# Kernel tuning notes

Hardware: AMD Instinct MI355X
Metric: run time of the kernel (lower is better)

Reference implementation:

```python
import jax, jax.numpy as jnp
import numpy as np

CLS_THR = 0.7      # cls_threshold
NMS_THR = 0.7      # nms_threshold
MAX_OUT = 100      # nms_max_outputs
MIN_SIZE = 3.0     # min_size_threshold


def setup_inputs() -> dict:
    key = jax.random.key(0)
    k1, k2 = jax.random.split(key)
    B, H, W, A = 1, 128, 128, 9
    img_h = img_w = 2048
    # build valid pixel-space boxes [y1,x1,y2,x2] with y2>y1, x2>x1
    r = jax.random.uniform(k1, (B, H, W, A, 4), dtype=jnp.float32)
    y1 = r[..., 0] * (img_h - 200.0)
    x1 = r[..., 1] * (img_w - 200.0)
    y2 = y1 + 1.0 + r[..., 2] * 199.0
    x2 = x1 + 1.0 + r[..., 3] * 199.0
    proposals = jnp.stack([y1, x1, y2, x2], axis=-1).reshape(B, H, W, A * 4)
    cls_score = jax.random.normal(k2, (B, H, W, A * 2), dtype=jnp.float32) * 2.0
    return {"proposals": proposals, "cls_score": cls_score,
            "image_h": img_h, "image_w": img_w}


def reference(proposals, cls_score, image_h, image_w):
    B, H, W = proposals.shape[0], proposals.shape[1], proposals.shape[2]
    A = proposals.shape[3] // 4
    boxes = proposals.reshape(-1, 4)                       # [N,4] yxyx, pixels
    prob = jax.nn.softmax(cls_score.reshape(B, H, W, A, 2), axis=-1)
    score0 = prob[..., 0].reshape(-1)                      # [N] objectness
    # threshold mask (tf boolean_mask replaced by fixed-shape invalidation)
    active0 = jnp.where(score0 > CLS_THR, score0, -1.0)
    areas = (boxes[:, 2] - boxes[:, 0]) * (boxes[:, 3] - boxes[:, 1])

    def nms_step(active, _):
        idx = jnp.argmax(active)
        ok = active[idx] > 0.0                             # any box left?
        b = boxes[idx]
        yy1 = jnp.maximum(b[0], boxes[:, 0])
        xx1 = jnp.maximum(b[1], boxes[:, 1])
        yy2 = jnp.minimum(b[2], boxes[:, 2])
        xx2 = jnp.minimum(b[3], boxes[:, 3])
        inter = jnp.maximum(yy2 - yy1, 0.0) * jnp.maximum(xx2 - xx1, 0.0)
        iou = inter / (areas + areas[idx] - inter + 1e-9)
        active = jnp.where(iou > NMS_THR, -1.0, active)
        active = active.at[idx].set(-1.0)
        return active, (idx, ok)

    _, (idxs, oks) = jax.lax.scan(nms_step, active0, None, length=MAX_OUT)
    sel_boxes = boxes[idxs]                                # [100,4]
    sel_cls = score0[idxs]                                 # [100]
    # remove_small_proposals: h,w from yxyx -> yxhw
    hgt = sel_boxes[:, 2] - sel_boxes[:, 0]
    wid = sel_boxes[:, 3] - sel_boxes[:, 1]
    keep = oks & (hgt > MIN_SIZE) & (wid > MIN_SIZE)
    sel_boxes = jnp.where(keep[:, None], sel_boxes, 0.0)
    sel_cls = jnp.where(keep, sel_cls, 0.0)
    # format == 'percentage': exact pixel coords -> fraction of image
    scale = jnp.array([image_h, image_w, image_h, image_w], dtype=jnp.float32)
    sel_boxes = (sel_boxes / scale)[None]                  # [1,100,4]
    return sel_boxes, sel_cls[None]                        # [1,100]
```

## Files before the change

### kernel.cpp

```cpp
#include <hip/hip_runtime.h>


#define CLS_THR 0.7f
#define NMS_THR 0.7f
#define MAX_OUT 100
#define MIN_SZ  3.0f

#define N_CAP      147456
#define BASE_BITS  0x3F333334u
#define BIN_SHIFT  9
#define NBINS      9831
#define HIST_WORDS 10240
#define PAD_WORD   10000
#define CTR_WORD   10100
#define TARGET     160u
#define CAP        512
#define CHUNK      128
#define BUCKET_NB  1024
#define BUCKET_LO  (NBINS - BUCKET_NB)
#define BCAP       64

__device__ __forceinline__ float softmax0(float l0, float l1) {
    float m  = fmaxf(l0, l1);
    float e0 = expf(l0 - m);
    float e1 = expf(l1 - m);
    return e0 / (e0 + e1);
}

__device__ __forceinline__ unsigned int ld_dev_u32(const unsigned int* p) {
    return __hip_atomic_load(p, __ATOMIC_RELAXED, __HIP_MEMORY_SCOPE_AGENT);
}
__device__ __forceinline__ unsigned long long ld_dev_u64(const unsigned long long* p) {
    return __hip_atomic_load(p, __ATOMIC_RELAXED, __HIP_MEMORY_SCOPE_AGENT);
}
__device__ __forceinline__ void st_dev_u64(unsigned long long* p, unsigned long long v) {
    __hip_atomic_store(p, v, __ATOMIC_RELAXED, __HIP_MEMORY_SCOPE_AGENT);
}
__device__ __forceinline__ unsigned long long pack2f(float a, float b) {
    return ((unsigned long long)__float_as_uint(b) << 32) | __float_as_uint(a);
}

__launch_bounds__(256)
__global__ void fused_kernel(const float4* __restrict__ boxes,
                             const float4* __restrict__ cls,
                             unsigned int* hist,
                             unsigned long long* bucket,
                             const int* __restrict__ ph, const int* __restrict__ pw,
                             float* __restrict__ out, int N, int nblocks)
{
    __shared__ unsigned long long s_kbuf[CAP];
    __shared__ unsigned long long s_sorted[CAP];
    __shared__ float4 s_bbox[CAP];
    __shared__ unsigned int s_binof[CAP];
    __shared__ unsigned int s_sup[CHUNK][4];
    __shared__ unsigned int s_rowflag[4];
    __shared__ unsigned int s_seedm[4];
    __shared__ unsigned int s_keep[4];
    __shared__ unsigned int s_gpack[CAP];
    __shared__ unsigned int s_goff[CAP];
    __shared__ unsigned int s_wsum[4];
    __shared__ float  s_klist[MAX_OUT][5];
    __shared__ float4 s_kbox[MAX_OUT];
    __shared__ float  s_karea[MAX_OUT];
    __shared__ int s_cbin, s_ov, s_kept, s_ne, s_last, s_cutT;
    __shared__ unsigned int s_M, s_cnt;

    const int tid  = threadIdx.x;
    const int lane = tid & 63;
    const int wave = tid >> 6;

    const unsigned int X = hist[PAD_WORD];

    {
        int t = blockIdx.x * 256 + tid;
        int i = t * 2;
        if (i < N) {
            float4 v  = cls[t];
            float4 b0 = boxes[i];
            float4 b1 = (i + 1 < N) ? boxes[i + 1] : b0;
            float p0 = softmax0(v.x, v.y);
            float p1 = (i + 1 < N) ? softmax0(v.z, v.w) : 0.0f;
            if (p0 > CLS_THR) {
                unsigned int b = __float_as_uint(p0);
                int bin = (int)((b - BASE_BITS) >> BIN_SHIFT);
                unsigned int slot = atomicAdd(&hist[bin], 1u) - X;
                if (bin >= BUCKET_LO && slot < BCAP) {
                    size_t ba = ((size_t)(bin - BUCKET_LO) * BCAP + slot) * 3;
                    st_dev_u64(&bucket[ba],
                        ((unsigned long long)b << 32) | (unsigned int)(~i));
                    st_dev_u64(&bucket[ba + 1], pack2f(b0.x, b0.y));
                    st_dev_u64(&bucket[ba + 2], pack2f(b0.z, b0.w));
                }
            }
            if (p1 > CLS_THR) {
                unsigned int b = __float_as_uint(p1);
                int bin = (int)((b - BASE_BITS) >> BIN_SHIFT);
                unsigned int slot = atomicAdd(&hist[bin], 1u) - X;
                if (bin >= BUCKET_LO && slot < BCAP) {
                    size_t ba = ((size_t)(bin - BUCKET_LO) * BCAP + slot) * 3;
                    st_dev_u64(&bucket[ba],
                        ((unsigned long long)b << 32) | (unsigned int)(~(i + 1)));
                    st_dev_u64(&bucket[ba + 1], pack2f(b1.x, b1.y));
                    st_dev_u64(&bucket[ba + 2], pack2f(b1.z, b1.w));
                }
            }
        }
    }
    asm volatile("s_waitcnt vmcnt(0)" ::: "memory");
    __syncthreads();
    if (tid == 0) {
        unsigned int old = atomicAdd(&hist[CTR_WORD], 1u);
        s_last = (old - X == (unsigned int)(nblocks - 1)) ? 1 : 0;
    }
    __syncthreads();
    if (!s_last) return;

    const float img_h = (float)(*ph);
    const float img_w = (float)(*pw);

    int kept = 0;
    int hi = NBINS;
    bool done = false;

    while (!done) {
        if (tid == 0) { s_cutT = -1; s_ov = 0; s_cnt = 0u; s_ne = 0; }
        __syncthreads();

        bool usefast = false;
        unsigned int h_reg = 0u, cum_reg = 0u;

        if (hi == NBINS) {
            int b = NBINS - 1 - tid;
            h_reg = ld_dev_u32(&hist[b]) - X;
            unsigned int pref = h_reg;
            #pragma unroll
            for (int o = 1; o < 64; o <<= 1) {
                unsigned int t2 = __shfl_up(pref, o);
                if (lane >= o) pref += t2;
            }
            if (lane == 63) s_wsum[wave] = pref;
            __syncthreads();
            unsigned int cum = pref;
            for (int q = 0; q < wave; ++q) cum += s_wsum[q];
            cum_reg = cum;
            if (cum >= TARGET && cum - h_reg < TARGET) {
                s_cutT = tid; s_M = cum; s_cbin = b;
            }
            __syncthreads();
            int cutT = s_cutT;
            if (cutT >= 0) {
                if (tid <= cutT && h_reg > BCAP) s_ov = 1;
                __syncthreads();
                usefast = (!s_ov) && (s_M <= 256u);
                if (usefast) {
                    if (tid <= cutT && h_reg > 0u) {
                        unsigned int off = cum_reg - h_reg;
                        unsigned int rb  = (unsigned int)(NBINS - 1 - tid - BUCKET_LO);
                        for (unsigned int s = 0; s < h_reg; ++s)
                            if (off + s < CAP) s_binof[off + s] = (rb << 6) | s;
                    }
                    __syncthreads();
                    unsigned int M = s_M;
                    unsigned long long key = 0ull;
                    float4 bx = make_float4(0.f, 0.f, 0.f, 0.f);
                    if ((unsigned int)tid < M) {
                        unsigned int bs = s_binof[tid];
                        size_t ba = ((size_t)(bs >> 6) * BCAP + (bs & 63u)) * 3;
                        key = ld_dev_u64(&bucket[ba]);
                        unsigned long long w1 = ld_dev_u64(&bucket[ba + 1]);
                        unsigned long long w2 = ld_dev_u64(&bucket[ba + 2]);
                        bx.x = __uint_as_float((unsigned int)w1);
                        bx.y = __uint_as_float((unsigned int)(w1 >> 32));
                        bx.z = __uint_as_float((unsigned int)w2);
                        bx.w = __uint_as_float((unsigned int)(w2 >> 32));
                        s_kbuf[tid] = key;
                    }
                    __syncthreads();
                    if ((unsigned int)tid < M) {
                        unsigned int rank = 0u;
                        #pragma unroll 8
                        for (unsigned int j = 0; j < M; ++j)
                            rank += (s_kbuf[j] > key) ? 1u : 0u;
                        s_sorted[rank] = key;
                        s_bbox[rank]   = bx;
                    }
                    __syncthreads();
                }
            } else {
                __syncthreads();
            }
        }

        if (!usefast) {
            if (wave == 0) {
                int pos = hi; unsigned int run = 0u; int cb = -1;
                unsigned int M = 0u; int ov = 0;
                while (pos > 0) {
                    int b = pos - 1 - lane;
                    unsigned int h = (b >= 0) ? (ld_dev_u32(&hist[b]) - X) : 0u;
                    unsigned int pref = h;
                    #pragma unroll
                    for (int o = 1; o < 64; o <<= 1) {
                        unsigned int t2 = __shfl_up(pref, o);
                        if (lane >= o) pref += t2;
                    }
                    unsigned int cum = run + pref;
                    unsigned long long okm = __ballot(b >= 0 && cum >= TARGET);
                    unsigned long long ovm = __ballot(b >= 0 && h > BCAP);
                    if (okm) {
                        int first = __builtin_ctzll(okm);
                        cb = pos - 1 - first;
                        M  = __shfl(cum, first);
                        unsigned long long lm = (first >= 63) ? ~0ull
                                              : ((1ull << (first + 1)) - 1ull);
                        if (ovm & lm) ov = 1;
                        break;
                    }
                    if (ovm) ov = 1;
                    run += __shfl(pref, 63);
                    pos -= 64;
                }
                if (cb < 0) { cb = 0; M = run; }
                if (lane == 0) { s_cbin = cb; s_M = M; s_ov = ov; }
            }
            __syncthreads();
        }

        const int cbin = s_cbin;
        const unsigned int M = s_M;
        if (M == 0u) break;
        const unsigned int M_eff = (M > CAP) ? CAP : M;

        if (!usefast) {
            const bool usebucket = (!s_ov) && (cbin >= BUCKET_LO);
            if (usebucket) {
                if (wave == 0) {
                    int pos = hi; unsigned int run = 0u; int ne = 0;
                    while (pos > cbin) {
                        int b = pos - 1 - lane;
                        unsigned int h = (b >= cbin) ? (ld_dev_u32(&hist[b]) - X) : 0u;
                        unsigned int pref = h;
                        #pragma unroll
                        for (int o = 1; o < 64; o <<= 1) {
                            unsigned int t2 = __shfl_up(pref, o);
                            if (lane >= o) pref += t2;
                        }
                        unsigned int offv = run + pref - h;
                        unsigned long long nzm = __ballot(h > 0u);
                        int slot = ne + __popcll(nzm & ((1ull << lane) - 1ull));
                        if (h > 0u && slot < CAP) {
                            s_gpack[slot] = ((unsigned int)b << 16) | h;
                            s_goff[slot]  = offv;
                        }
                        ne  += __popcll(nzm);
                        run += __shfl(pref, 63);
                        pos -= 64;
                    }
                    if (lane == 0) s_ne = ne;
                }
                __syncthreads();
                int ne = s_ne; if (ne > CAP) ne = CAP;
                for (int e = wave; e < ne; e += 4) {
                    unsigned int pk = s_gpack[e];
                    int b = (int)(pk >> 16);
                    unsigned int cnt = pk & 0xFFFFu;
                    unsigned int off = s_goff[e];
                    if (lane < (int)cnt && off + lane < CAP)
                        s_kbuf[off + lane] = ld_dev_u64(
                            &bucket[((size_t)(b - BUCKET_LO) * BCAP + lane) * 3]);
                }
            } else {
                unsigned int th_lo = BASE_BITS + ((unsigned int)cbin << BIN_SHIFT);
                unsigned int th_hi = BASE_BITS + ((unsigned int)hi   << BIN_SHIFT);
                int NV = N >> 1;
                for (int basei = 0; basei < NV; basei += 256 * 8) {
                    float4 v[8];
                    #pragma unroll
                    for (int u = 0; u < 8; ++u) {
                        int i4 = basei + u * 256 + tid;
                        v[u] = (i4 < NV) ? cls[i4]
                                         : make_float4(0.f, 0.f, 0.f, 0.f);
                    }
                    #pragma unroll
                    for (int u = 0; u < 8; ++u) {
                        int i0 = (basei + u * 256 + tid) * 2;
                        float p0 = softmax0(v[u].x, v[u].y);
                        float p1 = softmax0(v[u].z, v[u].w);
                        if (p0 > CLS_THR) {
                            unsigned int b = __float_as_uint(p0);
                            if (b >= th_lo && b < th_hi) {
                                unsigned int sl = atomicAdd(&s_cnt, 1u);
                                if (sl < CAP)
                                    s_kbuf[sl] = ((unsigned long long)b << 32)
                                               | (unsigned int)(~i0);
                            }
                        }
                        if (p1 > CLS_THR) {
                            unsigned int b = __float_as_uint(p1);
                            if (b >= th_lo && b < th_hi) {
                                unsigned int sl = atomicAdd(&s_cnt, 1u);
                                if (sl < CAP)
                                    s_kbuf[sl] = ((unsigned long long)b << 32)
                                               | (unsigned int)(~(i0 + 1));
                            }
                        }
                    }
                }
            }
            __syncthreads();
            for (unsigned int t = tid; t < M_eff; t += 256) {
                unsigned long long kt = s_kbuf[t];
                unsigned int rank = 0u;
                #pragma unroll 8
                for (unsigned int j = 0; j < M_eff; ++j)
                    rank += (s_kbuf[j] > kt) ? 1u : 0u;
                s_sorted[rank] = kt;
            }
            __syncthreads();
            for (unsigned int t = tid; t < M_eff; t += 256) {
                int idx = (int)(~(unsigned int)s_sorted[t]);
                s_bbox[t] = boxes[idx];
            }
            __syncthreads();
        }

        int base = 0;
        while (base < (int)M_eff && kept < MAX_OUT) {
            int C = (int)M_eff - base; if (C > CHUNK) C = CHUNK;
            if (tid < CHUNK) { s_sup[tid][0] = 0u; s_sup[tid][1] = 0u;
                               s_sup[tid][2] = 0u; s_sup[tid][3] = 0u; }
            if (tid < 4) { s_rowflag[tid] = 0u; s_seedm[tid] = 0u;
                           s_keep[tid] = 0u; }
            __syncthreads();

            if (kept > 0 && (tid & 127) < C) {
                int i = tid & 127;
                float4 cb = s_bbox[base + i];
                float ca = (cb.z - cb.x) * (cb.w - cb.y);
                bool sup = false;
                for (int j = (tid >> 7); j < kept; j += 2) {
                    float4 kb = s_kbox[j];
                    float yy1 = fmaxf(cb.x, kb.x), xx1 = fmaxf(cb.y, kb.y);
                    float yy2 = fminf(cb.z, kb.z), xx2 = fminf(cb.w, kb.w);
                    float it = fmaxf(yy2 - yy1, 0.f) * fmaxf(xx2 - xx1, 0.f);
                    sup = sup ||
                        (it / (ca + s_karea[j] - it + 1e-9f) > NMS_THR);
                }
                if (sup) atomicOr(&s_seedm[i >> 5], 1u << (i & 31));
            }
            for (int d = 1 + wave; d < C; d += 4) {
                #pragma unroll
                for (int half = 0; half < 2; ++half) {
                    int i = lane + half * 64;
                    if (i + d < C) {
                        float4 a  = s_bbox[base + i];
                        float4 b2 = s_bbox[base + i + d];
                        float aa = (a.z - a.x) * (a.w - a.y);
                        float ab = (b2.z - b2.x) * (b2.w - b2.y);
                        float yy1 = fmaxf(a.x, b2.x), xx1 = fmaxf(a.y, b2.y);
                        float yy2 = fminf(a.z, b2.z), xx2 = fminf(a.w, b2.w);
                        float it = fmaxf(yy2 - yy1, 0.f) * fmaxf(xx2 - xx1, 0.f);
                        if (it / (aa + ab - it + 1e-9f) > NMS_THR) {
                            int j = i + d;
                            atomicOr(&s_sup[i][j >> 5], 1u << (j & 31));
                            atomicOr(&s_rowflag[i >> 5], 1u << (i & 31));
                        }
                    }
                }
            }
            __syncthreads();

            if (wave == 0) {
                unsigned int ku[4] = {0u, 0u, 0u, 0u};
                unsigned int mg[4] = {s_seedm[0], s_seedm[1],
                                      s_seedm[2], s_seedm[3]};
                int k = kept;
                #pragma unroll
                for (int g = 0; g < 4; ++g) {
                    int lo = g * 32;
                    if (lo >= C || k >= MAX_OUT) continue;
                    int cg = C - lo; if (cg > 32) cg = 32;
                    unsigned int vmask = (cg >= 32) ? 0xFFFFFFFFu
                                        : ((1u << cg) - 1u);
                    unsigned int rem = vmask & ~mg[g];
                    while (rem && k < MAX_OUT) {
                        unsigned int flagged = rem & s_rowflag[g];
                        unsigned int pre; bool applyRow = false; int fb = 0;
                        if (!flagged) pre = rem;
                        else {
                            fb = __builtin_ctz(flagged); applyRow = true;
                            pre = rem & ((fb == 31) ? 0xFFFFFFFFu
                                                    : ((2u << fb) - 1u));
                        }
                        int c2 = __popc(pre);
                        int need = MAX_OUT - k;
                        if (c2 > need) {
                            while (c2 > need) {
                                pre &= ~(0x80000000u >> __builtin_clz(pre));
                                --c2;
                            }
                            ku[g] |= pre; k = MAX_OUT; break;
                        }
                        ku[g] |= pre; k += c2;
                        rem &= ~pre;
                        if (applyRow) {
                            int i = lo + fb;
                            mg[0] |= s_sup[i][0]; mg[1] |= s_sup[i][1];
                            mg[2] |= s_sup[i][2]; mg[3] |= s_sup[i][3];
                            rem &= ~mg[g];
                        }
                    }
                }
                if (lane == 0) {
                    s_keep[0] = ku[0]; s_keep[1] = ku[1];
                    s_keep[2] = ku[2]; s_keep[3] = ku[3];
                    s_kept = k;
                }
            }
            __syncthreads();
            int prevkept = kept;
            kept = s_kept;

            if (tid < C) {
                int w = tid >> 5, bp = tid & 31;
                unsigned int kw = s_keep[w];
                if ((kw >> bp) & 1u) {
                    int pre = __popc(kw & ((1u << bp) - 1u));
                    for (int q = 0; q < w; ++q) pre += __popc(s_keep[q]);
                    int slot = prevkept + pre;
                    float4 bb = s_bbox[base + tid];
                    s_klist[slot][0] = bb.x; s_klist[slot][1] = bb.y;
                    s_klist[slot][2] = bb.z; s_klist[slot][3] = bb.w;
                    s_klist[slot][4] = __uint_as_float(
                        (unsigned int)(s_sorted[base + tid] >> 32));
                    s_kbox[slot]  = bb;
                    s_karea[slot] = (bb.z - bb.x) * (bb.w - bb.y);
                }
            }
            __syncthreads();
            base += C;
        }

        done = (kept >= MAX_OUT) || (cbin == 0);
        hi = cbin;
    }

    __syncthreads();
    for (int j = tid; j < 4 * MAX_OUT + MAX_OUT; j += 256) {
        float val = 0.0f;
        if (j < 4 * MAX_OUT) {
            int k = j >> 2, cc = j & 3;
            if (k < kept) {
                float h = s_klist[k][2] - s_klist[k][0];
                float w = s_klist[k][3] - s_klist[k][1];
                if (h > MIN_SZ && w > MIN_SZ) {
                    float scale = (cc == 0 || cc == 2) ? img_h : img_w;
                    val = s_klist[k][cc] / scale;
                }
            }
        } else {
            int k = j - 4 * MAX_OUT;
            if (k < kept) {
                float h = s_klist[k][2] - s_klist[k][0];
                float w = s_klist[k][3] - s_klist[k][1];
                if (h > MIN_SZ && w > MIN_SZ) val = s_klist[k][4];
            }
        }
        out[j] = val;
    }
}

extern "C" void kernel_launch(void* const* d_in, const int* in_sizes, int n_in,
                              void* d_out, int out_size, void* d_ws, size_t ws_size,
                              hipStream_t stream) {
    const float* proposals = (const float*)d_in[0];
    const float* cls       = (const float*)d_in[1];
    const int*   ph        = (const int*)d_in[2];
    const int*   pw        = (const int*)d_in[3];
    float*       out       = (float*)d_out;

    int N = in_sizes[0] / 4;
    if (N > N_CAP) N = N_CAP;

    char* ws = (char*)d_ws;
    unsigned long long* bucket = (unsigned long long*)ws;
    unsigned int* hist = (unsigned int*)(ws + (size_t)BUCKET_NB * BCAP * 3 * 8);

    int nblocks = (N / 2 + 255) / 256;
    fused_kernel<<<nblocks, 256, 0, stream>>>(
        (const float4*)proposals, (const float4*)cls, hist, bucket,
        ph, pw, out, N, nblocks);
}
```

Measured before the change: 85.65 us.

## Store only score keys in buckets, reload boxes lazily, use 512-thread blocks

The first pass no longer reads box coordinates for every anchor or writes them into the global bucket; buckets now hold only the packed score and index key. The tail block fetches the box from the original proposals array by index once a candidate is selected. Block size grows from 256 to 512 threads, and the wave-strided loops in the single-block NMS tail are adjusted to match. This removes a large share of the streaming global reads and bucket stores. The cost is an extra dependent global load per candidate in the tail, plus new risk that code still assuming 4 waves breaks.

Result: faster. 80.16 us (-6.4%).

```diff
diff --git a/kernel.cpp b/kernel.cpp
--- a/kernel.cpp
+++ b/kernel.cpp
@@ -19,6 +19,8 @@
 #define BUCKET_NB  1024
 #define BUCKET_LO  (NBINS - BUCKET_NB)
 #define BCAP       64
+#define NTHR       512
+#define NBLK       144
 
 __device__ __forceinline__ float softmax0(float l0, float l1) {
     float m  = fmaxf(l0, l1);
@@ -36,11 +38,8 @@
 __device__ __forceinline__ void st_dev_u64(unsigned long long* p, unsigned long long v) {
     __hip_atomic_store(p, v, __ATOMIC_RELAXED, __HIP_MEMORY_SCOPE_AGENT);
 }
-__device__ __forceinline__ unsigned long long pack2f(float a, float b) {
-    return ((unsigned long long)__float_as_uint(b) << 32) | __float_as_uint(a);
-}
-
-__launch_bounds__(256)
+
+__launch_bounds__(NTHR)
 __global__ void fused_kernel(const float4* __restrict__ boxes,
                              const float4* __restrict__ cls,
                              unsigned int* hist,
@@ -58,7 +57,7 @@
     __shared__ unsigned int s_keep[4];
     __shared__ unsigned int s_gpack[CAP];
     __shared__ unsigned int s_goff[CAP];
-    __shared__ unsigned int s_wsum[4];
+    __shared__ unsigned int s_wsum[8];
     __shared__ float  s_klist[MAX_OUT][5];
     __shared__ float4 s_kbox[MAX_OUT];
     __shared__ float  s_karea[MAX_OUT];
@@ -72,37 +71,27 @@
     const unsigned int X = hist[PAD_WORD];
 
     {
-        int t = blockIdx.x * 256 + tid;
+        int t = blockIdx.x * NTHR + tid;
         int i = t * 2;
         if (i < N) {
-            float4 v  = cls[t];
-            float4 b0 = boxes[i];
-            float4 b1 = (i + 1 < N) ? boxes[i + 1] : b0;
+            float4 v = cls[t];
             float p0 = softmax0(v.x, v.y);
             float p1 = (i + 1 < N) ? softmax0(v.z, v.w) : 0.0f;
             if (p0 > CLS_THR) {
                 unsigned int b = __float_as_uint(p0);
                 int bin = (int)((b - BASE_BITS) >> BIN_SHIFT);
                 unsigned int slot = atomicAdd(&hist[bin], 1u) - X;
-                if (bin >= BUCKET_LO && slot < BCAP) {
-                    size_t ba = ((size_t)(bin - BUCKET_LO) * BCAP + slot) * 3;
-                    st_dev_u64(&bucket[ba],
+                if (bin >= BUCKET_LO && slot < BCAP)
+                    st_dev_u64(&bucket[(size_t)(bin - BUCKET_LO) * BCAP + slot],
                         ((unsigned long long)b << 32) | (unsigned int)(~i));
-                    st_dev_u64(&bucket[ba + 1], pack2f(b0.x, b0.y));
-                    st_dev_u64(&bucket[ba + 2], pack2f(b0.z, b0.w));
-                }
             }
             if (p1 > CLS_THR) {
                 unsigned int b = __float_as_uint(p1);
                 int bin = (int)((b - BASE_BITS) >> BIN_SHIFT);
                 unsigned int slot = atomicAdd(&hist[bin], 1u) - X;
-                if (bin >= BUCKET_LO && slot < BCAP) {
-                    size_t ba = ((size_t)(bin - BUCKET_LO) * BCAP + slot) * 3;
-                    st_dev_u64(&bucket[ba],
+                if (bin >= BUCKET_LO && slot < BCAP)
+                    st_dev_u64(&bucket[(size_t)(bin - BUCKET_LO) * BCAP + slot],
                         ((unsigned long long)b << 32) | (unsigned int)(~(i + 1)));
-                    st_dev_u64(&bucket[ba + 1], pack2f(b1.x, b1.y));
-                    st_dev_u64(&bucket[ba + 2], pack2f(b1.z, b1.w));
-                }
             }
         }
     }
@@ -131,20 +120,22 @@
 
         if (hi == NBINS) {
             int b = NBINS - 1 - tid;
-            h_reg = ld_dev_u32(&hist[b]) - X;
+            if (tid < 256) h_reg = ld_dev_u32(&hist[b]) - X;
             unsigned int pref = h_reg;
             #pragma unroll
             for (int o = 1; o < 64; o <<= 1) {
                 unsigned int t2 = __shfl_up(pref, o);
                 if (lane >= o) pref += t2;
             }
-            if (lane == 63) s_wsum[wave] = pref;
-            __syncthreads();
-            unsigned int cum = pref;
-            for (int q = 0; q < wave; ++q) cum += s_wsum[q];
-            cum_reg = cum;
-            if (cum >= TARGET && cum - h_reg < TARGET) {
-                s_cutT = tid; s_M = cum; s_cbin = b;
+            if (lane == 63 && wave < 4) s_wsum[wave] = pref;
+            __syncthreads();
+            if (tid < 256) {
+                unsigned int cum = pref;
+                for (int q = 0; q < wave; ++q) cum += s_wsum[q];
+                cum_reg = cum;
+                if (cum >= TARGET && cum - h_reg < TARGET) {
+                    s_cutT = tid; s_M = cum; s_cbin = b;
+                }
             }
             __syncthreads();
             int cutT = s_cutT;
@@ -162,21 +153,15 @@
                     __syncthreads();
                     unsigned int M = s_M;
                     unsigned long long key = 0ull;
-                    float4 bx = make_float4(0.f, 0.f, 0.f, 0.f);
                     if ((unsigned int)tid < M) {
                         unsigned int bs = s_binof[tid];
-                        size_t ba = ((size_t)(bs >> 6) * BCAP + (bs & 63u)) * 3;
-                        key = ld_dev_u64(&bucket[ba]);
-                        unsigned long long w1 = ld_dev_u64(&bucket[ba + 1]);
-                        unsigned long long w2 = ld_dev_u64(&bucket[ba + 2]);
-                        bx.x = __uint_as_float((unsigned int)w1);
-                        bx.y = __uint_as_float((unsigned int)(w1 >> 32));
-                        bx.z = __uint_as_float((unsigned int)w2);
-                        bx.w = __uint_as_float((unsigned int)(w2 >> 32));
+                        key = ld_dev_u64(&bucket[(size_t)(bs >> 6) * BCAP + (bs & 63u)]);
                         s_kbuf[tid] = key;
                     }
                     __syncthreads();
                     if ((unsigned int)tid < M) {
+                        int idx = (int)(~(unsigned int)key);
+                        float4 bx = boxes[idx];
                         unsigned int rank = 0u;
                         #pragma unroll 8
                         for (unsigned int j = 0; j < M; ++j)
@@ -260,30 +245,30 @@
                 }
                 __syncthreads();
                 int ne = s_ne; if (ne > CAP) ne = CAP;
-                for (int e = wave; e < ne; e += 4) {
+                for (int e = wave; e < ne; e += 8) {
                     unsigned int pk = s_gpack[e];
                     int b = (int)(pk >> 16);
                     unsigned int cnt = pk & 0xFFFFu;
                     unsigned int off = s_goff[e];
                     if (lane < (int)cnt && off + lane < CAP)
                         s_kbuf[off + lane] = ld_dev_u64(
-                            &bucket[((size_t)(b - BUCKET_LO) * BCAP + lane) * 3]);
+                            &bucket[(size_t)(b - BUCKET_LO) * BCAP + lane]);
                 }
             } else {
                 unsigned int th_lo = BASE_BITS + ((unsigned int)cbin << BIN_SHIFT);
                 unsigned int th_hi = BASE_BITS + ((unsigned int)hi   << BIN_SHIFT);
                 int NV = N >> 1;
-                for (int basei = 0; basei < NV; basei += 256 * 8) {
+                for (int basei = 0; basei < NV; basei += NTHR * 8) {
                     float4 v[8];
                     #pragma unroll
                     for (int u = 0; u < 8; ++u) {
-                        int i4 = basei + u * 256 + tid;
+                        int i4 = basei + u * NTHR + tid;
                         v[u] = (i4 < NV) ? cls[i4]
                                          : make_float4(0.f, 0.f, 0.f, 0.f);
                     }
                     #pragma unroll
                     for (int u = 0; u < 8; ++u) {
-                        int i0 = (basei + u * 256 + tid) * 2;
+                        int i0 = (basei + u * NTHR + tid) * 2;
                         float p0 = softmax0(v[u].x, v[u].y);
                         float p1 = softmax0(v[u].z, v[u].w);
                         if (p0 > CLS_THR) {
@@ -308,7 +293,7 @@
                 }
             }
             __syncthreads();
-            for (unsigned int t = tid; t < M_eff; t += 256) {
+            for (unsigned int t = tid; t < M_eff; t += NTHR) {
                 unsigned long long kt = s_kbuf[t];
                 unsigned int rank = 0u;
                 #pragma unroll 8
@@ -317,7 +302,7 @@
                 s_sorted[rank] = kt;
             }
             __syncthreads();
-            for (unsigned int t = tid; t < M_eff; t += 256) {
+            for (unsigned int t = tid; t < M_eff; t += NTHR) {
                 int idx = (int)(~(unsigned int)s_sorted[t]);
                 s_bbox[t] = boxes[idx];
             }
@@ -338,7 +323,7 @@
                 float4 cb = s_bbox[base + i];
                 float ca = (cb.z - cb.x) * (cb.w - cb.y);
                 bool sup = false;
-                for (int j = (tid >> 7); j < kept; j += 2) {
+                for (int j = (tid >> 7); j < kept; j += 4) {
                     float4 kb = s_kbox[j];
                     float yy1 = fmaxf(cb.x, kb.x), xx1 = fmaxf(cb.y, kb.y);
                     float yy2 = fminf(cb.z, kb.z), xx2 = fminf(cb.w, kb.w);
@@ -348,7 +333,7 @@
                 }
                 if (sup) atomicOr(&s_seedm[i >> 5], 1u << (i & 31));
             }
-            for (int d = 1 + wave; d < C; d += 4) {
+            for (int d = 1 + wave; d < C; d += 8) {
                 #pragma unroll
                 for (int half = 0; half < 2; ++half) {
                     int i = lane + half * 64;
@@ -446,7 +431,7 @@
     }
 
     __syncthreads();
-    for (int j = tid; j < 4 * MAX_OUT + MAX_OUT; j += 256) {
+    for (int j = tid; j < 4 * MAX_OUT + MAX_OUT; j += NTHR) {
         float val = 0.0f;
         if (j < 4 * MAX_OUT) {
             int k = j >> 2, cc = j & 3;
@@ -484,10 +469,10 @@
 
     char* ws = (char*)d_ws;
     unsigned long long* bucket = (unsigned long long*)ws;
-    unsigned int* hist = (unsigned int*)(ws + (size_t)BUCKET_NB * BCAP * 3 * 8);
-
-    int nblocks = (N / 2 + 255) / 256;
-    fused_kernel<<<nblocks, 256, 0, stream>>>(
+    unsigned int* hist = (unsigned int*)(ws + (size_t)BUCKET_NB * BCAP * 8);
+
+    int nblocks = (N / 2 + NTHR - 1) / NTHR;
+    fused_kernel<<<nblocks, NTHR, 0, stream>>>(
         (const float4*)proposals, (const float4*)cls, hist, bucket,
         ph, pw, out, N, nblocks);
 }
```
